# Performance work log

Hardware: AMD Instinct MI355X
Metric: run time of the kernel (lower is better)

The kernel has to match this reference:

```python
import jax, jax.numpy as jnp
import numpy as np

N_NODES = 50000
N_EDGES = 800000
N_GRAPHS = 128
IN_F = 768
NHID = 64
HID2 = NHID * 2  # 128
N_CLS = 2


def setup_inputs() -> dict:
    key = jax.random.key(0)
    ks = jax.random.split(key, 16)
    s = lambda k, shp, fan: jax.random.normal(k, shp, jnp.float32) / np.sqrt(fan)
    return {
        "x": jax.random.normal(ks[0], (N_NODES, IN_F), jnp.float32),
        "edge_index": jax.random.randint(ks[1], (2, N_EDGES), 0, N_NODES, jnp.int64),
        "batch": jnp.sort(jax.random.randint(ks[2], (N_NODES,), 0, N_GRAPHS, jnp.int64)),
        "W1": s(ks[3], (IN_F, HID2), IN_F),
        "as1": s(ks[4], (HID2,), HID2),
        "ad1": s(ks[5], (HID2,), HID2),
        "b1": jnp.zeros((HID2,), jnp.float32),
        "W2": s(ks[6], (HID2, HID2), HID2),
        "as2": s(ks[7], (HID2,), HID2),
        "ad2": s(ks[8], (HID2,), HID2),
        "b2": jnp.zeros((HID2,), jnp.float32),
        "fc1_w": s(ks[9], (HID2, NHID), HID2),
        "fc1_b": jnp.zeros((NHID,), jnp.float32),
        "fc2_w": s(ks[10], (NHID, N_CLS), NHID),
        "fc2_b": jnp.zeros((N_CLS,), jnp.float32),
    }


def _gat_conv(x, W, a_src, a_dst, b, src, dst):
    # PyG GATConv, heads=1, self-loops already included in (src, dst).
    xw = x @ W                                   # [N, F_out]
    e_src = xw @ a_src                           # [N]
    e_dst = xw @ a_dst                           # [N]
    e = jax.nn.leaky_relu(e_src[src] + e_dst[dst], 0.2)   # [E]
    m = jax.ops.segment_max(e, dst, num_segments=N_NODES)  # per-dst max (stable softmax)
    num = jnp.exp(e - m[dst])
    den = jax.ops.segment_sum(num, dst, num_segments=N_NODES)
    alpha = num / den[dst]                       # [E]
    out = jax.ops.segment_sum(alpha[:, None] * xw[src], dst, num_segments=N_NODES)
    return out + b


def reference(x, edge_index, batch, W1, as1, ad1, b1, W2, as2, ad2, b2,
              fc1_w, fc1_b, fc2_w, fc2_b):
    # add self loops (PyG GATConv default add_self_loops=True)
    loops = jnp.arange(N_NODES, dtype=edge_index.dtype)
    src = jnp.concatenate([edge_index[0], loops])
    dst = jnp.concatenate([edge_index[1], loops])

    h = jax.nn.selu(_gat_conv(x, W1, as1, ad1, b1, src, dst))
    h = jax.nn.selu(_gat_conv(h, W2, as2, ad2, b2, src, dst))

    # global mean pool over graphs
    sums = jax.ops.segment_sum(h, batch, num_segments=N_GRAPHS)          # [G, HID2]
    cnts = jax.ops.segment_sum(jnp.ones((N_NODES,), h.dtype), batch, num_segments=N_GRAPHS)
    pooled = jax.nn.selu(sums / jnp.maximum(cnts, 1.0)[:, None])

    g = jax.nn.selu(pooled @ fc1_w + fc1_b)      # dropout is identity in eval mode
    logits = g @ fc2_w + fc2_b
    return jax.nn.log_softmax(logits, axis=-1)
```

## Files before the change

kernel.cpp:

```cpp
#include <hip/hip_runtime.h>
#include <math.h>

#define N_NODES  50000
#define N_EDGES  800000
#define E_TOT    (N_EDGES + N_NODES)
#define N_GRAPHS 128
#define IN_F     768
#define HID2     128
#define NHID     64

typedef __attribute__((ext_vector_type(8))) short bf16x8;
typedef __attribute__((ext_vector_type(4))) float f32x4;
typedef __attribute__((ext_vector_type(4))) unsigned short us4;

__device__ __forceinline__ float selu_f(float x) {
    const float alpha = 1.6732632423543772f;
    const float scale = 1.0507009873554805f;
    return scale * (x > 0.f ? x : alpha * (expf(x) - 1.f));
}

__device__ __forceinline__ unsigned short f2bf(float f) {
    unsigned u = __float_as_uint(f);
    u += 0x7FFFu + ((u >> 16) & 1u);
    return (unsigned short)(u >> 16);
}
__device__ __forceinline__ float bf2f(unsigned short b) {
    return __uint_as_float(((unsigned)b) << 16);
}

__global__ void setup_k(const float* __restrict__ W1, const float* __restrict__ W2,
                        unsigned short* __restrict__ Wt1, unsigned short* __restrict__ Wt2,
                        unsigned* __restrict__ deg) {
    int i = blockIdx.x * blockDim.x + threadIdx.x;
    if (i < N_NODES) deg[i] = 0u;
    if (i < 128 * IN_F) {
        int n = i / IN_F, k = i - n * IN_F;
        Wt1[i] = f2bf(W1[(long)k * 128 + n]);
    }
    if (i < 128 * HID2) {
        int n = i >> 7, k = i & 127;
        Wt2[i] = f2bf(W2[(long)k * 128 + n]);
    }
}

#define LDA2 72
template<bool ABF16, bool OUTBF16>
__global__ __launch_bounds__(256) void gemm_mfma(
        const void* __restrict__ Av, const unsigned short* __restrict__ Bt,
        void* __restrict__ Cv, int M, int K) {
    __shared__ unsigned short As[64 * LDA2];
    __shared__ unsigned short Bs[128 * LDA2];
    const float* Af = (const float*)Av;
    const unsigned short* Ab = (const unsigned short*)Av;
    const int tid  = threadIdx.x;
    const int row0 = blockIdx.x * 64;
    const int w    = tid >> 6;
    const int lane = tid & 63;
    const int quad = lane >> 4;
    const int l16  = lane & 15;
    const int m_off = (w & 1) * 32;
    const int n_off = (w >> 1) * 64;

    f32x4 acc[2][4];
#pragma unroll
    for (int mi = 0; mi < 2; mi++)
#pragma unroll
        for (int ni = 0; ni < 4; ni++)
            acc[mi][ni] = (f32x4){0.f, 0.f, 0.f, 0.f};

    float4 aR[4];
    bf16x8 aRb[2];
    bf16x8 bR[4];
    if (ABF16) {
#pragma unroll
        for (int i = 0; i < 2; i++) {
            int p = tid + i * 256;
            int r = p >> 3, c8 = p & 7;
            int gr = row0 + r;
            aRb[i] = (gr < M) ? *(const bf16x8*)&Ab[(long)gr * K + c8 * 8]
                              : (bf16x8){0,0,0,0,0,0,0,0};
        }
    } else {
#pragma unroll
        for (int i = 0; i < 4; i++) {
            int p = tid + i * 256;
            int r = p >> 4, c4 = p & 15;
            int gr = row0 + r;
            aR[i] = (gr < M) ? *(const float4*)&Af[(long)gr * K + c4 * 4]
                             : make_float4(0.f, 0.f, 0.f, 0.f);
        }
    }
#pragma unroll
    for (int i = 0; i < 4; i++) {
        int c = tid + i * 256;
        int n = c >> 3, koff = (c & 7) * 8;
        bR[i] = *(const bf16x8*)&Bt[(long)n * K + koff];
    }

    for (int k0 = 0; k0 < K; k0 += 64) {
        if (ABF16) {
#pragma unroll
            for (int i = 0; i < 2; i++) {
                int p = tid + i * 256;
                int r = p >> 3, c8 = p & 7;
                *(bf16x8*)&As[r * LDA2 + c8 * 8] = aRb[i];
            }
        } else {
#pragma unroll
            for (int i = 0; i < 4; i++) {
                int p = tid + i * 256;
                int r = p >> 4, c4 = p & 15;
                us4 o;
                o.x = f2bf(aR[i].x); o.y = f2bf(aR[i].y);
                o.z = f2bf(aR[i].z); o.w = f2bf(aR[i].w);
                *(us4*)&As[r * LDA2 + c4 * 4] = o;
            }
        }
#pragma unroll
        for (int i = 0; i < 4; i++) {
            int c = tid + i * 256;
            int n = c >> 3, koff = (c & 7) * 8;
            *(bf16x8*)&Bs[n * LDA2 + koff] = bR[i];
        }
        __syncthreads();

        if (k0 + 64 < K) {
            int k1 = k0 + 64;
            if (ABF16) {
#pragma unroll
                for (int i = 0; i < 2; i++) {
                    int p = tid + i * 256;
                    int r = p >> 3, c8 = p & 7;
                    int gr = row0 + r;
                    aRb[i] = (gr < M) ? *(const bf16x8*)&Ab[(long)gr * K + k1 + c8 * 8]
                                      : (bf16x8){0,0,0,0,0,0,0,0};
                }
            } else {
#pragma unroll
                for (int i = 0; i < 4; i++) {
                    int p = tid + i * 256;
                    int r = p >> 4, c4 = p & 15;
                    int gr = row0 + r;
                    aR[i] = (gr < M) ? *(const float4*)&Af[(long)gr * K + k1 + c4 * 4]
                                     : make_float4(0.f, 0.f, 0.f, 0.f);
                }
            }
#pragma unroll
            for (int i = 0; i < 4; i++) {
                int c = tid + i * 256;
                int n = c >> 3, koff = (c & 7) * 8;
                bR[i] = *(const bf16x8*)&Bt[(long)n * K + k1 + koff];
            }
        }

        bf16x8 af[2][2], bfr[2][4];
#pragma unroll
        for (int kk = 0; kk < 2; kk++) {
#pragma unroll
            for (int mi = 0; mi < 2; mi++)
                af[kk][mi] = *(const bf16x8*)&As[(m_off + mi * 16 + l16) * LDA2 + kk * 32 + quad * 8];
#pragma unroll
            for (int ni = 0; ni < 4; ni++)
                bfr[kk][ni] = *(const bf16x8*)&Bs[(n_off + ni * 16 + l16) * LDA2 + kk * 32 + quad * 8];
        }
#pragma unroll
        for (int kk = 0; kk < 2; kk++)
#pragma unroll
            for (int mi = 0; mi < 2; mi++)
#pragma unroll
                for (int ni = 0; ni < 4; ni++)
                    acc[mi][ni] = __builtin_amdgcn_mfma_f32_16x16x32_bf16(
                        af[kk][mi], bfr[kk][ni], acc[mi][ni], 0, 0, 0);
        __syncthreads();
    }

#pragma unroll
    for (int mi = 0; mi < 2; mi++)
#pragma unroll
        for (int r = 0; r < 4; r++) {
            int row = row0 + m_off + mi * 16 + quad * 4 + r;
            if (row < M) {
                if (OUTBF16) {
                    unsigned short* C16 = (unsigned short*)Cv;
#pragma unroll
                    for (int ni = 0; ni < 4; ni++)
                        C16[(long)row * 128 + n_off + ni * 16 + l16] = f2bf(acc[mi][ni][r]);
                } else {
                    float* Cf = (float*)Cv;
#pragma unroll
                    for (int ni = 0; ni < 4; ni++)
                        Cf[(long)row * 128 + n_off + ni * 16 + l16] = acc[mi][ni][r];
                }
            }
        }
}

__global__ void node_e(const unsigned short* __restrict__ xw,
                       const float* __restrict__ a_s, const float* __restrict__ a_d,
                       float* __restrict__ e_src, float* __restrict__ e_dst) {
    int i = blockIdx.x * blockDim.x + threadIdx.x;
    if (i >= N_NODES) return;
    const bf16x8* row = (const bf16x8*)(xw + (long)i * HID2);
    float s = 0.f, d = 0.f;
#pragma unroll
    for (int j = 0; j < 16; j++) {
        bf16x8 v = row[j];
#pragma unroll
        for (int e = 0; e < 8; e++) {
            float f = bf2f((unsigned short)v[e]);
            s = fmaf(f, a_s[j * 8 + e], s);
            d = fmaf(f, a_d[j * 8 + e], d);
        }
    }
    e_src[i] = s;
    e_dst[i] = d;
}

__global__ void deg_hist(const int* __restrict__ ei, unsigned* __restrict__ deg) {
    int e = blockIdx.x * blockDim.x + threadIdx.x;
    if (e < N_EDGES) atomicAdd(&deg[ei[N_EDGES + e]], 1u);
}

__global__ __launch_bounds__(256) void scan_seed(const unsigned* __restrict__ deg,
                                                 unsigned* __restrict__ row_ptr,
                                                 unsigned* __restrict__ cursor,
                                                 unsigned* __restrict__ csr_src) {
    __shared__ unsigned psum_s[4];
    __shared__ unsigned wsum[4];
    int tid = threadIdx.x;
    int wid = tid >> 6, lane = tid & 63;
    int chunk0 = blockIdx.x * 256;

    unsigned psum = 0;
    for (int i = tid; i < chunk0; i += 256) psum += deg[i] + 1u;
    for (int o = 32; o; o >>= 1) psum += __shfl_xor(psum, o);
    if (lane == 0) psum_s[wid] = psum;

    int i = chunk0 + tid;
    unsigned v = (i < N_NODES) ? deg[i] + 1u : 0u;
    unsigned x = v;
    for (int o = 1; o < 64; o <<= 1) {
        unsigned y = __shfl_up(x, o);
        if (lane >= o) x += y;
    }
    if (lane == 63) wsum[wid] = x;
    __syncthreads();
    unsigned base = psum_s[0] + psum_s[1] + psum_s[2] + psum_s[3];
    unsigned wbase = 0;
    for (int k = 0; k < wid; k++) wbase += wsum[k];
    if (i < N_NODES) {
        unsigned rp = base + wbase + x - v;
        row_ptr[i] = rp;
        csr_src[rp] = (unsigned)i;
        cursor[i] = rp + 1;
        if (i == N_NODES - 1) row_ptr[N_NODES] = rp + v;
    }
}

__global__ void csr_scatter(const int* __restrict__ ei,
                            unsigned* __restrict__ cursor, unsigned* __restrict__ csr_src) {
    int e = blockIdx.x * blockDim.x + threadIdx.x;
    if (e >= N_EDGES) return;
    int d = ei[N_EDGES + e];
    unsigned p = atomicAdd(&cursor[d], 1u);
    csr_src[p] = (unsigned)ei[e];
}

template<bool OUTBF16>
__global__ __launch_bounds__(256) void gat_agg(
        const unsigned* __restrict__ row_ptr, const unsigned* __restrict__ csr_src,
        const float* __restrict__ e_src, const float* __restrict__ e_dst,
        const unsigned short* __restrict__ xw, const float* __restrict__ bias,
        void* __restrict__ outv) {
    __shared__ float2 buf[4][64];
    int wv = threadIdx.x >> 6;
    int node = blockIdx.x * 4 + wv;
    if (node >= N_NODES) return;
    int lane = threadIdx.x & 63;
    unsigned beg = row_ptr[node], end = row_ptr[node + 1];
    int deg = (int)(end - beg);
    float ed = e_dst[node];

    float a0 = 0.f, a1 = 0.f, den = 0.f;
    for (int base = 0; base < deg; base += 64) {
        int i = base + lane;
        float num = 0.f;
        unsigned s = 0u;
        if (i < deg) {
            s = csr_src[beg + i];
            float e = e_src[s] + ed;
            e = e > 0.f ? e : 0.2f * e;
            num = __expf(e);
            den += num;
        }
        float2 pk; pk.x = num; pk.y = __uint_as_float(s);
        buf[wv][lane] = pk;

        int cnt = deg - base; if (cnt > 64) cnt = 64;
        int j = 0;
        for (; j + 4 <= cnt; j += 4) {
            float2 p0 = buf[wv][j + 0];
            float2 p1 = buf[wv][j + 1];
            float2 p2 = buf[wv][j + 2];
            float2 p3 = buf[wv][j + 3];
            unsigned q0 = *(const unsigned*)&xw[(long)__float_as_uint(p0.y) * HID2 + lane * 2];
            unsigned q1 = *(const unsigned*)&xw[(long)__float_as_uint(p1.y) * HID2 + lane * 2];
            unsigned q2 = *(const unsigned*)&xw[(long)__float_as_uint(p2.y) * HID2 + lane * 2];
            unsigned q3 = *(const unsigned*)&xw[(long)__float_as_uint(p3.y) * HID2 + lane * 2];
            a0 = fmaf(p0.x, __uint_as_float(q0 << 16), a0);
            a1 = fmaf(p0.x, __uint_as_float(q0 & 0xffff0000u), a1);
            a0 = fmaf(p1.x, __uint_as_float(q1 << 16), a0);
            a1 = fmaf(p1.x, __uint_as_float(q1 & 0xffff0000u), a1);
            a0 = fmaf(p2.x, __uint_as_float(q2 << 16), a0);
            a1 = fmaf(p2.x, __uint_as_float(q2 & 0xffff0000u), a1);
            a0 = fmaf(p3.x, __uint_as_float(q3 << 16), a0);
            a1 = fmaf(p3.x, __uint_as_float(q3 & 0xffff0000u), a1);
        }
        for (; j < cnt; j++) {
            float2 p = buf[wv][j];
            unsigned q = *(const unsigned*)&xw[(long)__float_as_uint(p.y) * HID2 + lane * 2];
            a0 = fmaf(p.x, __uint_as_float(q << 16), a0);
            a1 = fmaf(p.x, __uint_as_float(q & 0xffff0000u), a1);
        }
    }
    for (int o = 32; o; o >>= 1) den += __shfl_xor(den, o);
    float inv = 1.f / den;
    float v0 = selu_f(fmaf(a0, inv, bias[lane * 2]));
    float v1 = selu_f(fmaf(a1, inv, bias[lane * 2 + 1]));
    if (OUTBF16) {
        unsigned* ob = (unsigned*)outv;
        ob[(long)node * 64 + lane] = ((unsigned)f2bf(v1) << 16) | (unsigned)f2bf(v0);
    } else {
        float* of = (float*)outv;
        of[(long)node * HID2 + lane * 2]     = v0;
        of[(long)node * HID2 + lane * 2 + 1] = v1;
    }
}

__global__ __launch_bounds__(256) void pool_graph(
        const float* __restrict__ h, const int* __restrict__ batch,
        float* __restrict__ pooled) {
    int g = blockIdx.x;
    int lo = 0, hi = N_NODES;
    while (lo < hi) { int mid = (lo + hi) >> 1; if (batch[mid] < g) lo = mid + 1; else hi = mid; }
    int start = lo;
    lo = start; hi = N_NODES;
    while (lo < hi) { int mid = (lo + hi) >> 1; if (batch[mid] < g + 1) lo = mid + 1; else hi = mid; }
    int end = lo;

    int f = threadIdx.x & 127, half = threadIdx.x >> 7;
    float acc = 0.f;
    for (int n = start + half; n < end; n += 2) acc += h[(long)n * HID2 + f];
    __shared__ float part[HID2];
    if (half == 0) part[f] = acc;
    __syncthreads();
    if (half == 1) {
        float tot = part[f] + acc;
        float c = (float)(end - start);
        c = c > 1.f ? c : 1.f;
        pooled[g * HID2 + f] = selu_f(tot / c);
    }
}

__global__ void fc1_k(const float* __restrict__ pooled, const float* __restrict__ w,
                      const float* __restrict__ b, float* __restrict__ g) {
    __shared__ float row[HID2];
    int gi = blockIdx.x, j = threadIdx.x;
    row[j] = pooled[gi * HID2 + j];
    row[j + 64] = pooled[gi * HID2 + 64 + j];
    __syncthreads();
    float acc = b[j];
#pragma unroll
    for (int k = 0; k < HID2; k++) acc = fmaf(row[k], w[k * NHID + j], acc);
    g[gi * NHID + j] = selu_f(acc);
}

__global__ void fc2_k(const float* __restrict__ g, const float* __restrict__ w,
                      const float* __restrict__ b, float* __restrict__ out) {
    int gi = blockIdx.x * blockDim.x + threadIdx.x;
    if (gi >= N_GRAPHS) return;
    float l0 = b[0], l1 = b[1];
#pragma unroll
    for (int k = 0; k < NHID; k++) {
        float v = g[gi * NHID + k];
        l0 = fmaf(v, w[k * 2 + 0], l0);
        l1 = fmaf(v, w[k * 2 + 1], l1);
    }
    float m = fmaxf(l0, l1);
    float lse = m + logf(expf(l0 - m) + expf(l1 - m));
    out[gi * 2 + 0] = l0 - lse;
    out[gi * 2 + 1] = l1 - lse;
}

extern "C" void kernel_launch(void* const* d_in, const int* in_sizes, int n_in,
                              void* d_out, int out_size, void* d_ws, size_t ws_size,
                              hipStream_t stream) {
    const float* x     = (const float*)d_in[0];
    const int*   ei    = (const int*)d_in[1];
    const int*   batch = (const int*)d_in[2];
    const float* W1    = (const float*)d_in[3];
    const float* as1   = (const float*)d_in[4];
    const float* ad1   = (const float*)d_in[5];
    const float* b1    = (const float*)d_in[6];
    const float* W2    = (const float*)d_in[7];
    const float* as2   = (const float*)d_in[8];
    const float* ad2   = (const float*)d_in[9];
    const float* b2    = (const float*)d_in[10];
    const float* fc1w  = (const float*)d_in[11];
    const float* fc1b  = (const float*)d_in[12];
    const float* fc2w  = (const float*)d_in[13];
    const float* fc2b  = (const float*)d_in[14];
    float* out = (float*)d_out;

    const long NH = (long)N_NODES * HID2;
    unsigned short* xwb = (unsigned short*)d_ws;
    unsigned short* h1b = xwb + NH;
    float*    B2      = (float*)(h1b + NH);
    float*    e_src   = B2 + NH;
    float*    e_dst   = e_src + N_NODES;
    unsigned* deg     = (unsigned*)(e_dst + N_NODES);
    unsigned* cursor  = deg + N_NODES;
    unsigned* row_ptr = cursor + N_NODES;
    unsigned* csr_src = row_ptr + N_NODES + 1;
    float*    pooled  = (float*)(csr_src + E_TOT);
    float*    g       = pooled + N_GRAPHS * HID2;
    unsigned short* Wt1 = (unsigned short*)(g + N_GRAPHS * NHID);
    unsigned short* Wt2 = Wt1 + 128 * IN_F;

    const int TB = 256;
    const int gNode = (N_NODES + TB - 1) / TB;
    const int gEdge = (N_EDGES + TB - 1) / TB;
    const int gGemm = (N_NODES + 63) / 64;
    const int gAgg  = (N_NODES + 3) / 4;

    setup_k<<<(128 * IN_F + TB - 1) / TB, TB, 0, stream>>>(W1, W2, Wt1, Wt2, deg);
    deg_hist<<<gEdge, TB, 0, stream>>>(ei, deg);
    scan_seed<<<gNode, TB, 0, stream>>>(deg, row_ptr, cursor, csr_src);
    csr_scatter<<<gEdge, TB, 0, stream>>>(ei, cursor, csr_src);

    gemm_mfma<false, true><<<gGemm, 256, 0, stream>>>(x, Wt1, xwb, N_NODES, IN_F);
    node_e<<<gNode, TB, 0, stream>>>(xwb, as1, ad1, e_src, e_dst);
    gat_agg<true><<<gAgg, 256, 0, stream>>>(row_ptr, csr_src, e_src, e_dst, xwb, b1, h1b);

    gemm_mfma<true, true><<<gGemm, 256, 0, stream>>>(h1b, Wt2, xwb, N_NODES, HID2);
    node_e<<<gNode, TB, 0, stream>>>(xwb, as2, ad2, e_src, e_dst);
    gat_agg<false><<<gAgg, 256, 0, stream>>>(row_ptr, csr_src, e_src, e_dst, xwb, b2, B2);

    pool_graph<<<N_GRAPHS, 256, 0, stream>>>(B2, batch, pooled);
    fc1_k<<<N_GRAPHS, NHID, 0, stream>>>(pooled, fc1w, fc1b, g);
    fc2_k<<<1, 128, 0, stream>>>(g, fc2w, fc2b, out);
}
```

Baseline: 537.0 us.

## Fuse attention logits into GEMM epilogue, vectorize aggregation, fuse pooling head

Attention logits e_src/e_dst are now computed in the MFMA GEMM epilogue with shuffles and atomicAdd across the two column-half waves, which removes the separate node_e kernel and its re-read of xw. The aggregation kernel now splits each wave into two halves, each handling alternate edges and loading 4 bf16 features with a uint2 load, then combines the halves with a shuffle. The pooling, fc1 and fc2 kernels are merged into one per-graph kernel. In exchange, the logit buffers must be zeroed in setup, atomics are added, and the logits now come from fp32 accumulators rather than bf16-rounded outputs.

```diff
diff --git a/kernel.cpp b/kernel.cpp
--- a/kernel.cpp
+++ b/kernel.cpp
@@ -24,15 +24,20 @@
     u += 0x7FFFu + ((u >> 16) & 1u);
     return (unsigned short)(u >> 16);
 }
-__device__ __forceinline__ float bf2f(unsigned short b) {
-    return __uint_as_float(((unsigned)b) << 16);
-}
+__device__ __forceinline__ float bflo(unsigned q) { return __uint_as_float(q << 16); }
+__device__ __forceinline__ float bfhi(unsigned q) { return __uint_as_float(q & 0xffff0000u); }
 
 __global__ void setup_k(const float* __restrict__ W1, const float* __restrict__ W2,
                         unsigned short* __restrict__ Wt1, unsigned short* __restrict__ Wt2,
-                        unsigned* __restrict__ deg) {
+                        unsigned* __restrict__ deg,
+                        float* __restrict__ es1, float* __restrict__ ed1,
+                        float* __restrict__ es2, float* __restrict__ ed2) {
     int i = blockIdx.x * blockDim.x + threadIdx.x;
-    if (i < N_NODES) deg[i] = 0u;
+    if (i < N_NODES) {
+        deg[i] = 0u;
+        es1[i] = 0.f; ed1[i] = 0.f;
+        es2[i] = 0.f; ed2[i] = 0.f;
+    }
     if (i < 128 * IN_F) {
         int n = i / IN_F, k = i - n * IN_F;
         Wt1[i] = f2bf(W1[(long)k * 128 + n]);
@@ -47,7 +52,9 @@
 template<bool ABF16, bool OUTBF16>
 __global__ __launch_bounds__(256) void gemm_mfma(
         const void* __restrict__ Av, const unsigned short* __restrict__ Bt,
-        void* __restrict__ Cv, int M, int K) {
+        void* __restrict__ Cv, int M, int K,
+        const float* __restrict__ a_s, const float* __restrict__ a_d,
+        float* __restrict__ es, float* __restrict__ ed) {
     __shared__ unsigned short As[64 * LDA2];
     __shared__ unsigned short Bs[128 * LDA2];
     const float* Af = (const float*)Av;
@@ -174,12 +181,36 @@
         __syncthreads();
     }
 
+    float as_v[4], ad_v[4];
+#pragma unroll
+    for (int ni = 0; ni < 4; ni++) {
+        int col = n_off + ni * 16 + l16;
+        as_v[ni] = a_s[col];
+        ad_v[ni] = a_d[col];
+    }
+
 #pragma unroll
     for (int mi = 0; mi < 2; mi++)
 #pragma unroll
         for (int r = 0; r < 4; r++) {
             int row = row0 + m_off + mi * 16 + quad * 4 + r;
+            float ps = 0.f, pd = 0.f;
+#pragma unroll
+            for (int ni = 0; ni < 4; ni++) {
+                float v = acc[mi][ni][r];
+                ps = fmaf(v, as_v[ni], ps);
+                pd = fmaf(v, ad_v[ni], pd);
+            }
+#pragma unroll
+            for (int o = 1; o < 16; o <<= 1) {
+                ps += __shfl_xor(ps, o);
+                pd += __shfl_xor(pd, o);
+            }
             if (row < M) {
+                if (l16 == 0) {
+                    atomicAdd(es + row, ps);
+                    atomicAdd(ed + row, pd);
+                }
                 if (OUTBF16) {
                     unsigned short* C16 = (unsigned short*)Cv;
 #pragma unroll
@@ -193,27 +224,6 @@
                 }
             }
         }
-}
-
-__global__ void node_e(const unsigned short* __restrict__ xw,
-                       const float* __restrict__ a_s, const float* __restrict__ a_d,
-                       float* __restrict__ e_src, float* __restrict__ e_dst) {
-    int i = blockIdx.x * blockDim.x + threadIdx.x;
-    if (i >= N_NODES) return;
-    const bf16x8* row = (const bf16x8*)(xw + (long)i * HID2);
-    float s = 0.f, d = 0.f;
-#pragma unroll
-    for (int j = 0; j < 16; j++) {
-        bf16x8 v = row[j];
-#pragma unroll
-        for (int e = 0; e < 8; e++) {
-            float f = bf2f((unsigned short)v[e]);
-            s = fmaf(f, a_s[j * 8 + e], s);
-            d = fmaf(f, a_d[j * 8 + e], d);
-        }
-    }
-    e_src[i] = s;
-    e_dst[i] = d;
 }
 
 __global__ void deg_hist(const int* __restrict__ ei, unsigned* __restrict__ deg) {
@@ -277,11 +287,14 @@
     int node = blockIdx.x * 4 + wv;
     if (node >= N_NODES) return;
     int lane = threadIdx.x & 63;
+    int half = lane >> 5;
+    int fl   = lane & 31;
     unsigned beg = row_ptr[node], end = row_ptr[node + 1];
     int deg = (int)(end - beg);
     float ed = e_dst[node];
-
-    float a0 = 0.f, a1 = 0.f, den = 0.f;
+    const unsigned short* xwf = xw + fl * 4;
+
+    float ax = 0.f, ay = 0.f, az = 0.f, aw = 0.f, den = 0.f;
     for (int base = 0; base < deg; base += 64) {
         int i = base + lane;
         float num = 0.f;
@@ -297,99 +310,102 @@
         buf[wv][lane] = pk;
 
         int cnt = deg - base; if (cnt > 64) cnt = 64;
-        int j = 0;
-        for (; j + 4 <= cnt; j += 4) {
-            float2 p0 = buf[wv][j + 0];
-            float2 p1 = buf[wv][j + 1];
-            float2 p2 = buf[wv][j + 2];
-            float2 p3 = buf[wv][j + 3];
-            unsigned q0 = *(const unsigned*)&xw[(long)__float_as_uint(p0.y) * HID2 + lane * 2];
-            unsigned q1 = *(const unsigned*)&xw[(long)__float_as_uint(p1.y) * HID2 + lane * 2];
-            unsigned q2 = *(const unsigned*)&xw[(long)__float_as_uint(p2.y) * HID2 + lane * 2];
-            unsigned q3 = *(const unsigned*)&xw[(long)__float_as_uint(p3.y) * HID2 + lane * 2];
-            a0 = fmaf(p0.x, __uint_as_float(q0 << 16), a0);
-            a1 = fmaf(p0.x, __uint_as_float(q0 & 0xffff0000u), a1);
-            a0 = fmaf(p1.x, __uint_as_float(q1 << 16), a0);
-            a1 = fmaf(p1.x, __uint_as_float(q1 & 0xffff0000u), a1);
-            a0 = fmaf(p2.x, __uint_as_float(q2 << 16), a0);
-            a1 = fmaf(p2.x, __uint_as_float(q2 & 0xffff0000u), a1);
-            a0 = fmaf(p3.x, __uint_as_float(q3 << 16), a0);
-            a1 = fmaf(p3.x, __uint_as_float(q3 & 0xffff0000u), a1);
-        }
-        for (; j < cnt; j++) {
-            float2 p = buf[wv][j];
-            unsigned q = *(const unsigned*)&xw[(long)__float_as_uint(p.y) * HID2 + lane * 2];
-            a0 = fmaf(p.x, __uint_as_float(q << 16), a0);
-            a1 = fmaf(p.x, __uint_as_float(q & 0xffff0000u), a1);
-        }
-    }
+        int steps = (cnt + 1) >> 1;
+        int t = 0;
+        for (; t + 4 <= steps; t += 4) {
+            float2 p0 = buf[wv][2 * (t + 0) + half];
+            float2 p1 = buf[wv][2 * (t + 1) + half];
+            float2 p2 = buf[wv][2 * (t + 2) + half];
+            float2 p3 = buf[wv][2 * (t + 3) + half];
+            uint2 q0 = *(const uint2*)&xwf[(long)__float_as_uint(p0.y) * HID2];
+            uint2 q1 = *(const uint2*)&xwf[(long)__float_as_uint(p1.y) * HID2];
+            uint2 q2 = *(const uint2*)&xwf[(long)__float_as_uint(p2.y) * HID2];
+            uint2 q3 = *(const uint2*)&xwf[(long)__float_as_uint(p3.y) * HID2];
+            ax = fmaf(p0.x, bflo(q0.x), ax); ay = fmaf(p0.x, bfhi(q0.x), ay);
+            az = fmaf(p0.x, bflo(q0.y), az); aw = fmaf(p0.x, bfhi(q0.y), aw);
+            ax = fmaf(p1.x, bflo(q1.x), ax); ay = fmaf(p1.x, bfhi(q1.x), ay);
+            az = fmaf(p1.x, bflo(q1.y), az); aw = fmaf(p1.x, bfhi(q1.y), aw);
+            ax = fmaf(p2.x, bflo(q2.x), ax); ay = fmaf(p2.x, bfhi(q2.x), ay);
+            az = fmaf(p2.x, bflo(q2.y), az); aw = fmaf(p2.x, bfhi(q2.y), aw);
+            ax = fmaf(p3.x, bflo(q3.x), ax); ay = fmaf(p3.x, bfhi(q3.x), ay);
+            az = fmaf(p3.x, bflo(q3.y), az); aw = fmaf(p3.x, bfhi(q3.y), aw);
+        }
+        for (; t < steps; t++) {
+            float2 p = buf[wv][2 * t + half];
+            uint2 q = *(const uint2*)&xwf[(long)__float_as_uint(p.y) * HID2];
+            ax = fmaf(p.x, bflo(q.x), ax); ay = fmaf(p.x, bfhi(q.x), ay);
+            az = fmaf(p.x, bflo(q.y), az); aw = fmaf(p.x, bfhi(q.y), aw);
+        }
+    }
+    ax += __shfl_xor(ax, 32); ay += __shfl_xor(ay, 32);
+    az += __shfl_xor(az, 32); aw += __shfl_xor(aw, 32);
     for (int o = 32; o; o >>= 1) den += __shfl_xor(den, o);
     float inv = 1.f / den;
-    float v0 = selu_f(fmaf(a0, inv, bias[lane * 2]));
-    float v1 = selu_f(fmaf(a1, inv, bias[lane * 2 + 1]));
-    if (OUTBF16) {
-        unsigned* ob = (unsigned*)outv;
-        ob[(long)node * 64 + lane] = ((unsigned)f2bf(v1) << 16) | (unsigned)f2bf(v0);
-    } else {
-        float* of = (float*)outv;
-        of[(long)node * HID2 + lane * 2]     = v0;
-        of[(long)node * HID2 + lane * 2 + 1] = v1;
-    }
-}
-
-__global__ __launch_bounds__(256) void pool_graph(
+    float v0 = selu_f(fmaf(ax, inv, bias[fl * 4 + 0]));
+    float v1 = selu_f(fmaf(ay, inv, bias[fl * 4 + 1]));
+    float v2 = selu_f(fmaf(az, inv, bias[fl * 4 + 2]));
+    float v3 = selu_f(fmaf(aw, inv, bias[fl * 4 + 3]));
+    if (half == 0) {
+        if (OUTBF16) {
+            uint2 o;
+            o.x = ((unsigned)f2bf(v1) << 16) | (unsigned)f2bf(v0);
+            o.y = ((unsigned)f2bf(v3) << 16) | (unsigned)f2bf(v2);
+            *(uint2*)((unsigned short*)outv + (long)node * HID2 + fl * 4) = o;
+        } else {
+            float4 o = make_float4(v0, v1, v2, v3);
+            *(float4*)((float*)outv + (long)node * HID2 + fl * 4) = o;
+        }
+    }
+}
+
+__global__ __launch_bounds__(256) void pool_head(
         const float* __restrict__ h, const int* __restrict__ batch,
-        float* __restrict__ pooled) {
+        const float* __restrict__ fc1w, const float* __restrict__ fc1b,
+        const float* __restrict__ fc2w, const float* __restrict__ fc2b,
+        float* __restrict__ out) {
+    __shared__ float pooled_s[HID2];
+    __shared__ float part[HID2];
+    __shared__ float g_s[NHID];
     int g = blockIdx.x;
     int lo = 0, hi = N_NODES;
     while (lo < hi) { int mid = (lo + hi) >> 1; if (batch[mid] < g) lo = mid + 1; else hi = mid; }
     int start = lo;
-    lo = start; hi = N_NODES;
+    hi = N_NODES;
     while (lo < hi) { int mid = (lo + hi) >> 1; if (batch[mid] < g + 1) lo = mid + 1; else hi = mid; }
     int end = lo;
 
     int f = threadIdx.x & 127, half = threadIdx.x >> 7;
     float acc = 0.f;
     for (int n = start + half; n < end; n += 2) acc += h[(long)n * HID2 + f];
-    __shared__ float part[HID2];
     if (half == 0) part[f] = acc;
     __syncthreads();
     if (half == 1) {
-        float tot = part[f] + acc;
         float c = (float)(end - start);
         c = c > 1.f ? c : 1.f;
-        pooled[g * HID2 + f] = selu_f(tot / c);
-    }
-}
-
-__global__ void fc1_k(const float* __restrict__ pooled, const float* __restrict__ w,
-                      const float* __restrict__ b, float* __restrict__ g) {
-    __shared__ float row[HID2];
-    int gi = blockIdx.x, j = threadIdx.x;
-    row[j] = pooled[gi * HID2 + j];
-    row[j + 64] = pooled[gi * HID2 + 64 + j];
+        pooled_s[f] = selu_f((part[f] + acc) / c);
+    }
     __syncthreads();
-    float acc = b[j];
-#pragma unroll
-    for (int k = 0; k < HID2; k++) acc = fmaf(row[k], w[k * NHID + j], acc);
-    g[gi * NHID + j] = selu_f(acc);
-}
-
-__global__ void fc2_k(const float* __restrict__ g, const float* __restrict__ w,
-                      const float* __restrict__ b, float* __restrict__ out) {
-    int gi = blockIdx.x * blockDim.x + threadIdx.x;
-    if (gi >= N_GRAPHS) return;
-    float l0 = b[0], l1 = b[1];
-#pragma unroll
-    for (int k = 0; k < NHID; k++) {
-        float v = g[gi * NHID + k];
-        l0 = fmaf(v, w[k * 2 + 0], l0);
-        l1 = fmaf(v, w[k * 2 + 1], l1);
-    }
-    float m = fmaxf(l0, l1);
-    float lse = m + logf(expf(l0 - m) + expf(l1 - m));
-    out[gi * 2 + 0] = l0 - lse;
-    out[gi * 2 + 1] = l1 - lse;
+    int j = threadIdx.x;
+    if (j < NHID) {
+        float a = fc1b[j];
+#pragma unroll
+        for (int k = 0; k < HID2; k++) a = fmaf(pooled_s[k], fc1w[k * NHID + j], a);
+        g_s[j] = selu_f(a);
+    }
+    __syncthreads();
+    if (j == 0) {
+        float l0 = fc2b[0], l1 = fc2b[1];
+#pragma unroll
+        for (int k = 0; k < NHID; k++) {
+            float v = g_s[k];
+            l0 = fmaf(v, fc2w[2 * k + 0], l0);
+            l1 = fmaf(v, fc2w[2 * k + 1], l1);
+        }
+        float m = fmaxf(l0, l1);
+        float lse = m + logf(expf(l0 - m) + expf(l1 - m));
+        out[g * 2 + 0] = l0 - lse;
+        out[g * 2 + 1] = l1 - lse;
+    }
 }
 
 extern "C" void kernel_launch(void* const* d_in, const int* in_sizes, int n_in,
@@ -416,15 +432,15 @@
     unsigned short* xwb = (unsigned short*)d_ws;
     unsigned short* h1b = xwb + NH;
     float*    B2      = (float*)(h1b + NH);
-    float*    e_src   = B2 + NH;
-    float*    e_dst   = e_src + N_NODES;
-    unsigned* deg     = (unsigned*)(e_dst + N_NODES);
+    float*    es1     = B2 + NH;
+    float*    ed1     = es1 + N_NODES;
+    float*    es2     = ed1 + N_NODES;
+    float*    ed2     = es2 + N_NODES;
+    unsigned* deg     = (unsigned*)(ed2 + N_NODES);
     unsigned* cursor  = deg + N_NODES;
     unsigned* row_ptr = cursor + N_NODES;
     unsigned* csr_src = row_ptr + N_NODES + 1;
-    float*    pooled  = (float*)(csr_src + E_TOT);
-    float*    g       = pooled + N_GRAPHS * HID2;
-    unsigned short* Wt1 = (unsigned short*)(g + N_GRAPHS * NHID);
+    unsigned short* Wt1 = (unsigned short*)(csr_src + E_TOT);
     unsigned short* Wt2 = Wt1 + 128 * IN_F;
 
     const int TB = 256;
@@ -433,20 +449,19 @@
     const int gGemm = (N_NODES + 63) / 64;
     const int gAgg  = (N_NODES + 3) / 4;
 
-    setup_k<<<(128 * IN_F + TB - 1) / TB, TB, 0, stream>>>(W1, W2, Wt1, Wt2, deg);
+    setup_k<<<(128 * IN_F + TB - 1) / TB, TB, 0, stream>>>(W1, W2, Wt1, Wt2, deg,
+                                                           es1, ed1, es2, ed2);
     deg_hist<<<gEdge, TB, 0, stream>>>(ei, deg);
     scan_seed<<<gNode, TB, 0, stream>>>(deg, row_ptr, cursor, csr_src);
     csr_scatter<<<gEdge, TB, 0, stream>>>(ei, cursor, csr_src);
 
-    gemm_mfma<false, true><<<gGemm, 256, 0, stream>>>(x, Wt1, xwb, N_NODES, IN_F);
-    node_e<<<gNode, TB, 0, stream>>>(xwb, as1, ad1, e_src, e_dst);
-    gat_agg<true><<<gAgg, 256, 0, stream>>>(row_ptr, csr_src, e_src, e_dst, xwb, b1, h1b);
-
-    gemm_mfma<true, true><<<gGemm, 256, 0, stream>>>(h1b, Wt2, xwb, N_NODES, HID2);
-    node_e<<<gNode, TB, 0, stream>>>(xwb, as2, ad2, e_src, e_dst);
-    gat_agg<false><<<gAgg, 256, 0, stream>>>(row_ptr, csr_src, e_src, e_dst, xwb, b2, B2);
-
-    pool_graph<<<N_GRAPHS, 256, 0, stream>>>(B2, batch, pooled);
-    fc1_k<<<N_GRAPHS, NHID, 0, stream>>>(pooled, fc1w, fc1b, g);
-    fc2_k<<<1, 128, 0, stream>>>(g, fc2w, fc2b, out);
-}
+    gemm_mfma<false, true><<<gGemm, 256, 0, stream>>>(x, Wt1, xwb, N_NODES, IN_F,
+                                                      as1, ad1, es1, ed1);
+    gat_agg<true><<<gAgg, 256, 0, stream>>>(row_ptr, csr_src, es1, ed1, xwb, b1, h1b);
+
+    gemm_mfma<true, true><<<gGemm, 256, 0, stream>>>(h1b, Wt2, xwb, N_NODES, HID2,
+                                                     as2, ad2, es2, ed2);
+    gat_agg<false><<<gAgg, 256, 0, stream>>>(row_ptr, csr_src, es2, ed2, xwb, b2, B2);
+
+    pool_head<<<N_GRAPHS, 256, 0, stream>>>(B2, batch, fc1w, fc1b, fc2w, fc2b, out);
+}
```

Result: faster. 521.6 us (-2.9%).
